# Optimization experiments

Hardware: AMD Instinct MI355X
Metric: run time of the kernel (lower is better)

The kernel has to match this reference:

```python
import jax, jax.numpy as jnp
import numpy as np
import math

B, N, D = 4, 1024, 1024
H = 16
HD = D // H          # 64
TOP_K = 64
NUM_STATIC = 32


def setup_inputs() -> dict:
    key = jax.random.key(0)
    ks = jax.random.split(key, 10)
    s = 1.0 / math.sqrt(D)  # ~ nn.Linear default init scale
    inp = {
        "x": jax.random.normal(ks[0], (B, N, D), dtype=jnp.float32),
        "Wq": jax.random.uniform(ks[1], (D, D), jnp.float32, -s, s),
        "bq": jax.random.uniform(ks[2], (D,), jnp.float32, -s, s),
        "Wk": jax.random.uniform(ks[3], (D, D), jnp.float32, -s, s),
        "bk": jax.random.uniform(ks[4], (D,), jnp.float32, -s, s),
        "Wv": jax.random.uniform(ks[5], (D, D), jnp.float32, -s, s),
        "bv": jax.random.uniform(ks[6], (D,), jnp.float32, -s, s),
        "Wo": jax.random.uniform(ks[7], (D, D), jnp.float32, -s, s),
        "bo": jax.random.uniform(ks[8], (D,), jnp.float32, -s, s),
        "static_keys": jax.random.normal(ks[9], (NUM_STATIC, D), dtype=jnp.float32),
    }
    return inp


def _heads(t):
    # [B, N, D] -> [B, H, N, HD]
    return t.reshape(B, N, H, HD).transpose(0, 2, 1, 3)


def reference(x, Wq, bq, Wk, bk, Wv, bv, Wo, bo, static_keys):
    Q = _heads(x @ Wq.T + bq)
    K = _heads(x @ Wk.T + bk)
    V = _heads(x @ Wv.T + bv)

    # Replace the first NUM_STATIC key slots with learned static keys.
    K_stat = static_keys.reshape(1, NUM_STATIC, H, HD).transpose(0, 2, 1, 3)  # [1,H,S,HD]
    K_stat = jnp.broadcast_to(K_stat, (B, H, NUM_STATIC, HD))
    K = jnp.concatenate([K_stat, K[:, :, NUM_STATIC:, :]], axis=2)  # [B,H,N,HD]

    scores = jnp.einsum("bhnd,bhmd->bhnm", Q, K) / math.sqrt(HD)  # [B,H,N,N]

    # top-k mask: keep top_k scores per query, -inf elsewhere
    top_scores, top_idx = jax.lax.top_k(scores, TOP_K)  # [B,H,N,K]
    bi = jnp.arange(B)[:, None, None, None]
    hi = jnp.arange(H)[None, :, None, None]
    ni = jnp.arange(N)[None, None, :, None]
    masked = jnp.full(scores.shape, -jnp.inf, dtype=scores.dtype)
    masked = masked.at[bi, hi, ni, top_idx].set(top_scores)

    attn = jax.nn.softmax(masked, axis=-1)
    out = jnp.einsum("bhnm,bhmd->bhnd", attn, V)  # [B,H,N,HD]
    out = out.transpose(0, 2, 1, 3).reshape(B, N, D)
    return out @ Wo.T + bo
```

## Files before the change

kernel.cpp:

```cpp
#include <hip/hip_runtime.h>

#define NSTAT 32
#define MAXSEL 76

typedef __attribute__((ext_vector_type(8))) short bf16x8_t;
typedef __attribute__((ext_vector_type(4))) float f32x4_t;

#define GLOAD_LDS16(g, l) \
    __builtin_amdgcn_global_load_lds((const __attribute__((address_space(1))) void*)(g), \
                                     (__attribute__((address_space(3))) void*)(l), 16, 0, 0)

__device__ __forceinline__ ushort rtn_bf16(float a) {
    unsigned u = __float_as_uint(a);
    return (ushort)((u + 0x7FFFu + ((u >> 16) & 1u)) >> 16);
}
__device__ __forceinline__ void limb2(float a, ushort& h, ushort& l) {
    ushort hh = rtn_bf16(a);
    float fh = __uint_as_float(((unsigned)hh) << 16);
    float r1 = a - fh;
    l = rtn_bf16(r1);
    h = hh;
}

__global__ __launch_bounds__(256)
void decomp_w_kernel(const float* __restrict__ Wq, const float* __restrict__ Wk,
                     const float* __restrict__ Wv, const float* __restrict__ Wo,
                     ushort* __restrict__ WLq, ushort* __restrict__ WoLb)
{
    const int m = blockIdx.y;
    const float* src = (m == 0) ? Wq : (m == 1) ? Wk : (m == 2) ? Wv : Wo;
    const int idx = blockIdx.x * 256 + threadIdx.x;
    const int e8 = idx * 8;
    const int row = e8 >> 10, k0 = e8 & 1023;
    const int kt = k0 >> 5, q = (k0 >> 3) & 3;
    const size_t doff = ((size_t)row << 10) + (size_t)(kt * 32) + (size_t)((q ^ (row & 3)) * 8);

    float4 v0 = *(const float4*)(src + e8);
    float4 v1 = *(const float4*)(src + e8 + 4);
    float f[8] = {v0.x, v0.y, v0.z, v0.w, v1.x, v1.y, v1.z, v1.w};

    const size_t Mi = (size_t)1 << 20;
    ushort h[8], l[8];
    #pragma unroll
    for (int e = 0; e < 8; ++e) limb2(f[e], h[e], l[e]);
    ushort* H = (m == 3) ? WoLb : WLq + (size_t)(m * 2) * Mi;
    ushort* L = H + Mi;
    *(ushort4*)(H + doff)     = make_ushort4(h[0],h[1],h[2],h[3]);
    *(ushort4*)(H + doff + 4) = make_ushort4(h[4],h[5],h[6],h[7]);
    *(ushort4*)(L + doff)     = make_ushort4(l[0],l[1],l[2],l[3]);
    *(ushort4*)(L + doff + 4) = make_ushort4(l[4],l[5],l[6],l[7]);
}

__global__ __launch_bounds__(256, 3)
void limb_gemm_kernel(const float* __restrict__ A,
                      const ushort* __restrict__ WLq, const ushort* __restrict__ WoLb,
                      const float* __restrict__ bq, const float* __restrict__ bk,
                      const float* __restrict__ bv, const float* __restrict__ bo,
                      const float* __restrict__ statk,
                      float* __restrict__ Qw, float* __restrict__ Vw,
                      ushort* __restrict__ KHo, ushort* __restrict__ KLo,
                      float* __restrict__ Cout, int is_out)
{
    __shared__ __align__(16) ushort Al[2][128][32];
    __shared__ __align__(16) ushort Bl[2][2][128][32];

    const int t = threadIdx.x;
    const int bx = blockIdx.x, by = blockIdx.y;
    const int mode = is_out ? 3 : (int)blockIdx.z;
    const int wc0 = bx * 128;
    const int arow0 = by * 128;

    const size_t Mi = (size_t)1 << 20;
    const ushort* BpH;
    const float* bias;
    if (mode == 0)      { BpH = WLq;          bias = bq; }
    else if (mode == 1) { BpH = WLq + 2*Mi;   bias = bk; }
    else if (mode == 2) { BpH = WLq + 4*Mi;   bias = bv; }
    else                { BpH = WoLb;         bias = bo; }
    const ushort* BpL = BpH + Mi;

    const int ll = t & 63, w = t >> 6;

    f32x4_t acc[4][4];
    #pragma unroll
    for (int i = 0; i < 4; ++i)
        #pragma unroll
        for (int j = 0; j < 4; ++j) acc[i][j] = (f32x4_t){0.f, 0.f, 0.f, 0.f};

    auto stageB = [&](int kt, int bb) {
        #pragma unroll
        for (int limb = 0; limb < 2; ++limb) {
            const ushort* src = limb ? BpL : BpH;
            #pragma unroll
            for (int call = 0; call < 2; ++call) {
                int chunk = (w * 2 + call) * 64 + ll;
                int eoff = chunk * 8;
                int row = eoff >> 5, qp = (eoff >> 3) & 3;
                const ushort* g = src + ((size_t)(wc0 + row) << 10) + kt * 32 + qp * 8;
                char* l = ((char*)&Bl[bb][limb][0][0]) + (w * 2 + call) * 1024;
                GLOAD_LDS16(g, l);
            }
        }
    };
    const int srow = t >> 1, skh = (t & 1) * 16;
    auto loadA = [&](int kt, float4* a4) {
        const float* p = A + (((size_t)(arow0 + srow)) << 10) + kt * 32 + skh;
        a4[0] = *(const float4*)(p + 0);
        a4[1] = *(const float4*)(p + 4);
        a4[2] = *(const float4*)(p + 8);
        a4[3] = *(const float4*)(p + 12);
    };
    auto writeA = [&](const float4* a4) {
        float f[16];
        #pragma unroll
        for (int i = 0; i < 4; ++i) {
            f[i*4+0] = a4[i].x; f[i*4+1] = a4[i].y; f[i*4+2] = a4[i].z; f[i*4+3] = a4[i].w;
        }
        ushort h[16], lo[16];
        #pragma unroll
        for (int e = 0; e < 16; ++e) limb2(f[e], h[e], lo[e]);
        const int sw = srow & 3;
        #pragma unroll
        for (int qq = 0; qq < 2; ++qq) {
            int q = (skh >> 3) + qq;
            int qo = (q ^ sw) * 8;
            bf16x8_t vH, vL;
            #pragma unroll
            for (int e = 0; e < 8; ++e) {
                vH[e] = (short)h[qq*8+e]; vL[e] = (short)lo[qq*8+e];
            }
            *(bf16x8_t*)&Al[0][srow][qo] = vH;
            *(bf16x8_t*)&Al[1][srow][qo] = vL;
        }
    };

    const int wr = (w >> 1) * 64, wcv = (w & 1) * 64;
    const int fr = ll & 15, kg = ll >> 4;

    auto compute = [&](int bb) {
        bf16x8_t af[4][2];
        #pragma unroll
        for (int i = 0; i < 4; ++i) {
            int row = wr + i * 16 + fr;
            int qo = (kg ^ (row & 3)) * 8;
            af[i][0] = *(const bf16x8_t*)&Al[0][row][qo];
            af[i][1] = *(const bf16x8_t*)&Al[1][row][qo];
        }
        #pragma unroll
        for (int j = 0; j < 4; ++j) {
            int row = wcv + j * 16 + fr;
            int qo = (kg ^ (row & 3)) * 8;
            bf16x8_t b0 = *(const bf16x8_t*)&Bl[bb][0][row][qo];
            bf16x8_t b1 = *(const bf16x8_t*)&Bl[bb][1][row][qo];
            #pragma unroll
            for (int i = 0; i < 4; ++i) {
                acc[i][j] = __builtin_amdgcn_mfma_f32_16x16x32_bf16(af[i][0], b0, acc[i][j], 0, 0, 0);
                acc[i][j] = __builtin_amdgcn_mfma_f32_16x16x32_bf16(af[i][0], b1, acc[i][j], 0, 0, 0);
                acc[i][j] = __builtin_amdgcn_mfma_f32_16x16x32_bf16(af[i][1], b0, acc[i][j], 0, 0, 0);
            }
        }
    };

    float4 a4[4];
    loadA(0, a4);
    writeA(a4);
    stageB(0, 0);
    __syncthreads();

    float4 a4n[4];
    for (int kt = 0; kt < 32; ++kt) {
        int bb = kt & 1;
        if (kt < 31) {
            stageB(kt + 1, bb ^ 1);
            loadA(kt + 1, a4n);
        }
        compute(bb);
        __syncthreads();
        if (kt < 31) writeA(a4n);
        __syncthreads();
    }

    #pragma unroll
    for (int i = 0; i < 4; ++i) {
        #pragma unroll
        for (int j = 0; j < 4; ++j) {
            int c = wc0 + wcv + j * 16 + (ll & 15);
            float bv_ = bias[c];
            #pragma unroll
            for (int q = 0; q < 4; ++q) {
                int gr = arow0 + wr + i * 16 + (kg) * 4 + q;
                float v = acc[i][j][q] + bv_;
                if (mode == 3) {
                    Cout[(size_t)gr * 1024 + c] = v;
                } else {
                    int b = gr >> 10, n = gr & 1023;
                    int h = c >> 6, d = c & 63;
                    size_t bhn = ((size_t)(b * 16 + h)) * 1024 + n;
                    if (mode == 1) {
                        if (n < NSTAT) v = statk[n * 1024 + c];
                        ushort kh, klo;
                        limb2(v, kh, klo);
                        size_t off = bhn * 64 + (size_t)(((d >> 3) ^ (n & 7)) * 8) + (d & 7);
                        KHo[off] = kh;
                        KLo[off] = klo;
                    } else {
                        float* Out = (mode == 0) ? Qw : Vw;
                        Out[bhn * 64 + d] = v;
                    }
                }
            }
        }
    }
}

__device__ __forceinline__ void radix_stage7(int* __restrict__ hist, int r, int l,
                                             const unsigned* __restrict__ ku,
                                             unsigned pref, unsigned mask, int shift,
                                             int tgt, int2* __restrict__ piv)
{
    #pragma unroll
    for (int b = 0; b < 8; ++b) hist[(l*8 + b)*33 + r] = 0;
    __syncthreads();
    #pragma unroll
    for (int j = 0; j < 64; ++j) {
        unsigned k = ku[j];
        if ((k & mask) == pref)
            atomicAdd(&hist[(int)((k >> shift) & 127u)*33 + r], 1);
    }
    __syncthreads();
    int seg = 0;
    #pragma unroll
    for (int b = 0; b < 8; ++b) seg += hist[(l*8 + b)*33 + r];
    int suf = seg;
    #pragma unroll
    for (int off = 1; off < 16; off <<= 1) {
        int v = __shfl_down(suf, off, 16);
        suf += (l + off < 16) ? v : 0;
    }
    const int above = suf - seg;
    if (above < tgt && above + seg >= tgt) {
        int c = above;
        #pragma unroll
        for (int b = 7; b >= 0; --b) {
            int h = hist[(l*8 + b)*33 + r];
            if (c + h >= tgt) { piv[r] = make_int2(l*8 + b, tgt - c); break; }
            c += h;
        }
    }
    __syncthreads();
}

__global__ __launch_bounds__(512, 4)
void attn_mfma_kernel(const float* __restrict__ Qw,
                      const ushort* __restrict__ KH, const ushort* __restrict__ KL,
                      const float* __restrict__ Vw, float* __restrict__ outp)
{
    __shared__ __align__(16) char pool[58368];
    __shared__ int2 piv[32];
    __shared__ int cnt[32];
    __shared__ float rowsum[32];

    ushort* Klds0 = (ushort*)pool;
    ushort* Klds1 = Klds0 + 8192;
    int* hist = (int*)pool;
    float (*Qs)[68]  = (float(*)[68])(pool + 32768);
    float (*sc)[132] = (float(*)[132])(pool + 41472);
    uint2 (*sel)[MAXSEL] = (uint2(*)[MAXSEL])(pool + 32768);

    const int t = threadIdx.x;
    const int bid0 = blockIdx.x;
    const int bid = (bid0 & 7) * 256 + (bid0 >> 3);
    const int qt = bid & 31;
    const int bh = bid >> 5;
    const int n0 = qt * 32;
    const float* Qbase = Qw + ((size_t)bh * 1024 + n0) * 64;
    const float* Vbase = Vw + (size_t)bh * 1024 * 64;
    const ushort* KHb = KH + (size_t)bh * 1024 * 64;
    const ushort* KLb = KL + (size_t)bh * 1024 * 64;

    const int ll = t & 63;
    const int w  = t >> 6;
    const int qh = w >> 2;
    const int kr = w & 3;
    const int r  = t >> 4, l = t & 15;

    {
        int q = t >> 4, dq = (t & 15) * 4;
        *(float4*)&Qs[q][dq] = *(const float4*)(Qbase + q * 64 + dq);
    }
    auto stageK = [&](int c) {
        const size_t cb = (size_t)c * 8192;
        #pragma unroll
        for (int i = 0; i < 2; ++i) {
            int boff = i * 8192 + w * 1024;
            GLOAD_LDS16(KHb + cb + boff / 2 + ll * 8, ((char*)Klds0) + boff);
            GLOAD_LDS16(KLb + cb + boff / 2 + ll * 8, ((char*)Klds1) + boff);
        }
    };
    stageK(0);
    if (t < 32) cnt[t] = 0;
    __syncthreads();

    bf16x8_t aH[2], aL[2];
    {
        const int arow = qh * 16 + (ll & 15), akg = ll >> 4;
        #pragma unroll
        for (int s = 0; s < 2; ++s) {
            const float* qp = &Qs[arow][s*32 + akg*8];
            float4 q0 = *(const float4*)qp;
            float4 q1 = *(const float4*)(qp + 4);
            float qv[8] = {q0.x,q0.y,q0.z,q0.w,q1.x,q1.y,q1.z,q1.w};
            #pragma unroll
            for (int j = 0; j < 8; ++j) {
                ushort hh, lo2;
                limb2(qv[j], hh, lo2);
                aH[s][j] = (short)hh; aL[s][j] = (short)lo2;
            }
        }
    }
    __syncthreads();

    unsigned ku[64];

    #pragma unroll
    for (int c = 0; c < 8; ++c) {
        #pragma unroll
        for (int tile = 0; tile < 2; ++tile) {
            const int m0 = kr * 32 + tile * 16;
            const int brow = m0 + (ll & 15);
            f32x4_t a_ = {0.f, 0.f, 0.f, 0.f};
            #pragma unroll
            for (int s = 0; s < 2; ++s) {
                int q2 = (s*4 + (ll >> 4)) ^ (brow & 7);
                int off = brow*64 + q2*8;
                bf16x8_t bH = *(const bf16x8_t*)&Klds0[off];
                bf16x8_t bL = *(const bf16x8_t*)&Klds1[off];
                a_ = __builtin_amdgcn_mfma_f32_16x16x32_bf16(aH[s], bH, a_, 0, 0, 0);
                a_ = __builtin_amdgcn_mfma_f32_16x16x32_bf16(aH[s], bL, a_, 0, 0, 0);
                a_ = __builtin_amdgcn_mfma_f32_16x16x32_bf16(aL[s], bH, a_, 0, 0, 0);
            }
            const int qr = qh * 16 + (ll >> 4) * 4;
            const int mcol = m0 + (ll & 15);
            sc[qr+0][mcol] = a_[0];
            sc[qr+1][mcol] = a_[1];
            sc[qr+2][mcol] = a_[2];
            sc[qr+3][mcol] = a_[3];
        }
        __syncthreads();

        if (c < 7) stageK(c + 1);
        {
            float4 v0 = *(const float4*)&sc[r][l*8];
            float4 v1 = *(const float4*)&sc[r][l*8 + 4];
            float vv[8] = {v0.x,v0.y,v0.z,v0.w,v1.x,v1.y,v1.z,v1.w};
            #pragma unroll
            for (int e = 0; e < 8; ++e) {
                float vc = fminf(fmaxf(vv[e], -31.9f), 31.9f);
                ku[c*8 + e] = (unsigned)(int)fmaf(vc, 32768.f, 1048576.f);
            }
        }
        __syncthreads();
    }

    int tgt = 64;
    radix_stage7(hist, r, l, ku, 0u, 0u, 14, tgt, piv);
    unsigned pref = (unsigned)piv[r].x << 14; tgt = piv[r].y;
    radix_stage7(hist, r, l, ku, pref, 0x1FC000u, 7, tgt, piv);
    pref |= (unsigned)piv[r].x << 7; tgt = piv[r].y;
    radix_stage7(hist, r, l, ku, pref, 0x1FFF80u, 0, tgt, piv);
    const unsigned thr = pref | (unsigned)piv[r].x;

    const unsigned bhi = thr + 2u;
    const unsigned blo = thr - 2u;
    #pragma unroll
    for (int j = 0; j < 64; ++j) {
        unsigned k = ku[j];
        if (k >= blo) {
            int slot = atomicAdd(&cnt[r], 1);
            if (slot < MAXSEL)
                sel[r][slot] = make_uint2((unsigned)((j >> 3)*128 + l*8 + (j & 7)), k);
        }
    }
    __syncthreads();

    {
        int cc = cnt[r]; cc = (cc < MAXSEL) ? cc : MAXSEL;
        int Dl = 0, ml = 0;
        for (int j = l; j < cc; j += 16) {
            unsigned k = sel[r][j].y;
            if (k > bhi) Dl++; else ml++;
        }
        #pragma unroll
        for (int off = 8; off; off >>= 1) {
            Dl += __shfl_xor(Dl, off, 16);
            ml += __shfl_xor(ml, off, 16);
        }
        const float frac = (float)(64 - Dl) / (float)ml;
        float ls = 0.f;
        for (int j = l; j < cc; j += 16) {
            uint2 p = sel[r][j];
            float wgt = __expf((float)(int)(p.y - thr) * 3.814697265625e-6f);
            if (p.y <= bhi) wgt *= frac;
            p.y = __float_as_uint(wgt);
            sel[r][j] = p;
            ls += wgt;
        }
        #pragma unroll
        for (int off = 8; off; off >>= 1) ls += __shfl_xor(ls, off, 16);
        if (l == 0) { rowsum[r] = ls; cnt[r] = cc; }
    }
    __syncthreads();

    {
        const int pr = t >> 4;
        const int d4 = (t & 15) * 4;
        const int bb = bh >> 4, hh = bh & 15;
        const int cc = cnt[pr];
        float4 a = make_float4(0.f, 0.f, 0.f, 0.f);
        int j = 0;
        for (; j + 1 < cc; j += 2) {
            uint2 p0 = sel[pr][j];
            uint2 p1 = sel[pr][j+1];
            float w0 = __uint_as_float(p0.y);
            float w1 = __uint_as_float(p1.y);
            float4 v0 = *(const float4*)(Vbase + (size_t)p0.x * 64 + d4);
            float4 v1 = *(const float4*)(Vbase + (size_t)p1.x * 64 + d4);
            a.x += w0 * v0.x + w1 * v1.x;
            a.y += w0 * v0.y + w1 * v1.y;
            a.z += w0 * v0.z + w1 * v1.z;
            a.w += w0 * v0.w + w1 * v1.w;
        }
        if (j < cc) {
            uint2 p = sel[pr][j];
            float wv = __uint_as_float(p.y);
            float4 v = *(const float4*)(Vbase + (size_t)p.x * 64 + d4);
            a.x += wv * v.x; a.y += wv * v.y; a.z += wv * v.z; a.w += wv * v.w;
        }
        float inv = 1.0f / rowsum[pr];
        a.x *= inv; a.y *= inv; a.z *= inv; a.w *= inv;
        *(float4*)(outp + ((size_t)bb * 1024 + (n0 + pr)) * 1024 + hh * 64 + d4) = a;
    }
}

extern "C" void kernel_launch(void* const* d_in, const int* in_sizes, int n_in,
                              void* d_out, int out_size, void* d_ws, size_t ws_size,
                              hipStream_t stream) {
    const float* x     = (const float*)d_in[0];
    const float* Wq    = (const float*)d_in[1];
    const float* bq    = (const float*)d_in[2];
    const float* Wk    = (const float*)d_in[3];
    const float* bk    = (const float*)d_in[4];
    const float* Wv    = (const float*)d_in[5];
    const float* bv    = (const float*)d_in[6];
    const float* Wo    = (const float*)d_in[7];
    const float* bo    = (const float*)d_in[8];
    const float* statk = (const float*)d_in[9];
    float* out = (float*)d_out;
    char* base = (char*)d_ws;

    const size_t MiB = (size_t)1 << 20;
    float*  Qw   = (float*)(base);
    float*  Vw   = (float*)(base + 16*MiB);
    ushort* KH   = (ushort*)(base + 32*MiB);
    ushort* KL   = (ushort*)(base + 40*MiB);
    ushort* WoLb = (ushort*)(base + 48*MiB);
    ushort* WLq  = (ushort*)(base + 52*MiB);
    float*  op   = (float*)(base + 52*MiB);

    dim3 gd(512, 4);
    decomp_w_kernel<<<gd, 256, 0, stream>>>(Wq, Wk, Wv, Wo, WLq, WoLb);

    dim3 g1(8, 32, 3);
    limb_gemm_kernel<<<g1, 256, 0, stream>>>(x, WLq, WoLb, bq, bk, bv, bo, statk,
                                             Qw, Vw, KH, KL, nullptr, 0);

    attn_mfma_kernel<<<2048, 512, 0, stream>>>(Qw, KH, KL, Vw, op);

    dim3 g2(8, 32);
    limb_gemm_kernel<<<g2, 256, 0, stream>>>(op, WLq, WoLb, bq, bk, bv, bo, statk,
                                             Qw, Vw, KH, KL, out, 1);
}
```

Baseline: 293.1 us.

## Halve attention query tile to 16 rows, doubling blocks and threads per row

Each attention block now handles 16 queries instead of 32, so the grid grows to 4096 blocks and 32 threads cooperate on each row's radix select, with half the keys per thread. This cuts per-thread register use (the key array drops from 64 to 32 entries) and LDS, so more blocks fit per CU. The weighted V accumulation is split across two half-groups and combined with a shuffle. In exchange, every K chunk is loaded from global memory twice as often per query, which raises K traffic and the per-block fixed overhead.

```diff
diff --git a/kernel.cpp b/kernel.cpp
--- a/kernel.cpp
+++ b/kernel.cpp
@@ -213,16 +213,16 @@
     }
 }
 
-__device__ __forceinline__ void radix_stage7(int* __restrict__ hist, int r, int l,
+__device__ __forceinline__ void radix_stage4(int* __restrict__ hist, int r, int l2,
                                              const unsigned* __restrict__ ku,
                                              unsigned pref, unsigned mask, int shift,
                                              int tgt, int2* __restrict__ piv)
 {
     #pragma unroll
-    for (int b = 0; b < 8; ++b) hist[(l*8 + b)*33 + r] = 0;
-    __syncthreads();
-    #pragma unroll
-    for (int j = 0; j < 64; ++j) {
+    for (int b = 0; b < 4; ++b) hist[(l2*4 + b)*33 + r] = 0;
+    __syncthreads();
+    #pragma unroll
+    for (int j = 0; j < 32; ++j) {
         unsigned k = ku[j];
         if ((k & mask) == pref)
             atomicAdd(&hist[(int)((k >> shift) & 127u)*33 + r], 1);
@@ -230,20 +230,20 @@
     __syncthreads();
     int seg = 0;
     #pragma unroll
-    for (int b = 0; b < 8; ++b) seg += hist[(l*8 + b)*33 + r];
+    for (int b = 0; b < 4; ++b) seg += hist[(l2*4 + b)*33 + r];
     int suf = seg;
     #pragma unroll
-    for (int off = 1; off < 16; off <<= 1) {
-        int v = __shfl_down(suf, off, 16);
-        suf += (l + off < 16) ? v : 0;
+    for (int off = 1; off < 32; off <<= 1) {
+        int v = __shfl_down(suf, off, 32);
+        suf += (l2 + off < 32) ? v : 0;
     }
     const int above = suf - seg;
     if (above < tgt && above + seg >= tgt) {
         int c = above;
         #pragma unroll
-        for (int b = 7; b >= 0; --b) {
-            int h = hist[(l*8 + b)*33 + r];
-            if (c + h >= tgt) { piv[r] = make_int2(l*8 + b, tgt - c); break; }
+        for (int b = 3; b >= 0; --b) {
+            int h = hist[(l2*4 + b)*33 + r];
+            if (c + h >= tgt) { piv[r] = make_int2(l2*4 + b, tgt - c); break; }
             c += h;
         }
     }
@@ -255,24 +255,24 @@
                       const ushort* __restrict__ KH, const ushort* __restrict__ KL,
                       const float* __restrict__ Vw, float* __restrict__ outp)
 {
-    __shared__ __align__(16) char pool[58368];
-    __shared__ int2 piv[32];
-    __shared__ int cnt[32];
-    __shared__ float rowsum[32];
+    __shared__ __align__(16) char pool[45568];
+    __shared__ int2 piv[16];
+    __shared__ int cnt[16];
+    __shared__ float rowsum[16];
 
     ushort* Klds0 = (ushort*)pool;
     ushort* Klds1 = Klds0 + 8192;
     int* hist = (int*)pool;
     float (*Qs)[68]  = (float(*)[68])(pool + 32768);
-    float (*sc)[132] = (float(*)[132])(pool + 41472);
+    float (*sc)[132] = (float(*)[132])(pool + 37120);
     uint2 (*sel)[MAXSEL] = (uint2(*)[MAXSEL])(pool + 32768);
 
     const int t = threadIdx.x;
     const int bid0 = blockIdx.x;
-    const int bid = (bid0 & 7) * 256 + (bid0 >> 3);
-    const int qt = bid & 31;
-    const int bh = bid >> 5;
-    const int n0 = qt * 32;
+    const int bid = (bid0 & 7) * 512 + (bid0 >> 3);
+    const int qt = bid & 63;
+    const int bh = bid >> 6;
+    const int n0 = qt * 16;
     const float* Qbase = Qw + ((size_t)bh * 1024 + n0) * 64;
     const float* Vbase = Vw + (size_t)bh * 1024 * 64;
     const ushort* KHb = KH + (size_t)bh * 1024 * 64;
@@ -280,11 +280,9 @@
 
     const int ll = t & 63;
     const int w  = t >> 6;
-    const int qh = w >> 2;
-    const int kr = w & 3;
-    const int r  = t >> 4, l = t & 15;
-
-    {
+    const int r  = t >> 5, l2 = t & 31;
+
+    if (t < 256) {
         int q = t >> 4, dq = (t & 15) * 4;
         *(float4*)&Qs[q][dq] = *(const float4*)(Qbase + q * 64 + dq);
     }
@@ -298,12 +296,12 @@
         }
     };
     stageK(0);
-    if (t < 32) cnt[t] = 0;
+    if (t < 16) cnt[t] = 0;
     __syncthreads();
 
     bf16x8_t aH[2], aL[2];
     {
-        const int arow = qh * 16 + (ll & 15), akg = ll >> 4;
+        const int arow = ll & 15, akg = ll >> 4;
         #pragma unroll
         for (int s = 0; s < 2; ++s) {
             const float* qp = &Qs[arow][s*32 + akg*8];
@@ -320,14 +318,12 @@
     }
     __syncthreads();
 
-    unsigned ku[64];
+    unsigned ku[32];
 
     #pragma unroll
     for (int c = 0; c < 8; ++c) {
-        #pragma unroll
-        for (int tile = 0; tile < 2; ++tile) {
-            const int m0 = kr * 32 + tile * 16;
-            const int brow = m0 + (ll & 15);
+        {
+            const int brow = w * 16 + (ll & 15);
             f32x4_t a_ = {0.f, 0.f, 0.f, 0.f};
             #pragma unroll
             for (int s = 0; s < 2; ++s) {
@@ -339,46 +335,44 @@
                 a_ = __builtin_amdgcn_mfma_f32_16x16x32_bf16(aH[s], bL, a_, 0, 0, 0);
                 a_ = __builtin_amdgcn_mfma_f32_16x16x32_bf16(aL[s], bH, a_, 0, 0, 0);
             }
-            const int qr = qh * 16 + (ll >> 4) * 4;
-            const int mcol = m0 + (ll & 15);
-            sc[qr+0][mcol] = a_[0];
-            sc[qr+1][mcol] = a_[1];
-            sc[qr+2][mcol] = a_[2];
-            sc[qr+3][mcol] = a_[3];
+            const int qr = (ll >> 4) * 4;
+            sc[qr+0][brow] = a_[0];
+            sc[qr+1][brow] = a_[1];
+            sc[qr+2][brow] = a_[2];
+            sc[qr+3][brow] = a_[3];
         }
         __syncthreads();
 
         if (c < 7) stageK(c + 1);
         {
-            float4 v0 = *(const float4*)&sc[r][l*8];
-            float4 v1 = *(const float4*)&sc[r][l*8 + 4];
-            float vv[8] = {v0.x,v0.y,v0.z,v0.w,v1.x,v1.y,v1.z,v1.w};
-            #pragma unroll
-            for (int e = 0; e < 8; ++e) {
+            float4 v4 = *(const float4*)&sc[r][l2*4];
+            float vv[4] = {v4.x, v4.y, v4.z, v4.w};
+            #pragma unroll
+            for (int e = 0; e < 4; ++e) {
                 float vc = fminf(fmaxf(vv[e], -31.9f), 31.9f);
-                ku[c*8 + e] = (unsigned)(int)fmaf(vc, 32768.f, 1048576.f);
+                ku[c*4 + e] = (unsigned)(int)fmaf(vc, 32768.f, 1048576.f);
             }
         }
         __syncthreads();
     }
 
     int tgt = 64;
-    radix_stage7(hist, r, l, ku, 0u, 0u, 14, tgt, piv);
+    radix_stage4(hist, r, l2, ku, 0u, 0u, 14, tgt, piv);
     unsigned pref = (unsigned)piv[r].x << 14; tgt = piv[r].y;
-    radix_stage7(hist, r, l, ku, pref, 0x1FC000u, 7, tgt, piv);
+    radix_stage4(hist, r, l2, ku, pref, 0x1FC000u, 7, tgt, piv);
     pref |= (unsigned)piv[r].x << 7; tgt = piv[r].y;
-    radix_stage7(hist, r, l, ku, pref, 0x1FFF80u, 0, tgt, piv);
+    radix_stage4(hist, r, l2, ku, pref, 0x1FFF80u, 0, tgt, piv);
     const unsigned thr = pref | (unsigned)piv[r].x;
 
     const unsigned bhi = thr + 2u;
     const unsigned blo = thr - 2u;
     #pragma unroll
-    for (int j = 0; j < 64; ++j) {
+    for (int j = 0; j < 32; ++j) {
         unsigned k = ku[j];
         if (k >= blo) {
             int slot = atomicAdd(&cnt[r], 1);
             if (slot < MAXSEL)
-                sel[r][slot] = make_uint2((unsigned)((j >> 3)*128 + l*8 + (j & 7)), k);
+                sel[r][slot] = make_uint2((unsigned)((j >> 2)*128 + l2*4 + (j & 3)), k);
         }
     }
     __syncthreads();
@@ -386,18 +380,18 @@
     {
         int cc = cnt[r]; cc = (cc < MAXSEL) ? cc : MAXSEL;
         int Dl = 0, ml = 0;
-        for (int j = l; j < cc; j += 16) {
+        for (int j = l2; j < cc; j += 32) {
             unsigned k = sel[r][j].y;
             if (k > bhi) Dl++; else ml++;
         }
         #pragma unroll
-        for (int off = 8; off; off >>= 1) {
-            Dl += __shfl_xor(Dl, off, 16);
-            ml += __shfl_xor(ml, off, 16);
+        for (int off = 16; off; off >>= 1) {
+            Dl += __shfl_xor(Dl, off, 32);
+            ml += __shfl_xor(ml, off, 32);
         }
         const float frac = (float)(64 - Dl) / (float)ml;
         float ls = 0.f;
-        for (int j = l; j < cc; j += 16) {
+        for (int j = l2; j < cc; j += 32) {
             uint2 p = sel[r][j];
             float wgt = __expf((float)(int)(p.y - thr) * 3.814697265625e-6f);
             if (p.y <= bhi) wgt *= frac;
@@ -406,39 +400,33 @@
             ls += wgt;
         }
         #pragma unroll
-        for (int off = 8; off; off >>= 1) ls += __shfl_xor(ls, off, 16);
-        if (l == 0) { rowsum[r] = ls; cnt[r] = cc; }
+        for (int off = 16; off; off >>= 1) ls += __shfl_xor(ls, off, 32);
+        if (l2 == 0) { rowsum[r] = ls; cnt[r] = cc; }
     }
     __syncthreads();
 
     {
-        const int pr = t >> 4;
+        const int pr = t >> 5;
+        const int h2 = (t >> 4) & 1;
         const int d4 = (t & 15) * 4;
         const int bb = bh >> 4, hh = bh & 15;
         const int cc = cnt[pr];
         float4 a = make_float4(0.f, 0.f, 0.f, 0.f);
-        int j = 0;
-        for (; j + 1 < cc; j += 2) {
-            uint2 p0 = sel[pr][j];
-            uint2 p1 = sel[pr][j+1];
-            float w0 = __uint_as_float(p0.y);
-            float w1 = __uint_as_float(p1.y);
-            float4 v0 = *(const float4*)(Vbase + (size_t)p0.x * 64 + d4);
-            float4 v1 = *(const float4*)(Vbase + (size_t)p1.x * 64 + d4);
-            a.x += w0 * v0.x + w1 * v1.x;
-            a.y += w0 * v0.y + w1 * v1.y;
-            a.z += w0 * v0.z + w1 * v1.z;
-            a.w += w0 * v0.w + w1 * v1.w;
-        }
-        if (j < cc) {
+        for (int j = h2; j < cc; j += 2) {
             uint2 p = sel[pr][j];
             float wv = __uint_as_float(p.y);
             float4 v = *(const float4*)(Vbase + (size_t)p.x * 64 + d4);
             a.x += wv * v.x; a.y += wv * v.y; a.z += wv * v.z; a.w += wv * v.w;
         }
-        float inv = 1.0f / rowsum[pr];
-        a.x *= inv; a.y *= inv; a.z *= inv; a.w *= inv;
-        *(float4*)(outp + ((size_t)bb * 1024 + (n0 + pr)) * 1024 + hh * 64 + d4) = a;
+        a.x += __shfl_xor(a.x, 16);
+        a.y += __shfl_xor(a.y, 16);
+        a.z += __shfl_xor(a.z, 16);
+        a.w += __shfl_xor(a.w, 16);
+        if (h2 == 0) {
+            float inv = 1.0f / rowsum[pr];
+            a.x *= inv; a.y *= inv; a.z *= inv; a.w *= inv;
+            *(float4*)(outp + ((size_t)bb * 1024 + (n0 + pr)) * 1024 + hh * 64 + d4) = a;
+        }
     }
 }
 
@@ -474,7 +462,7 @@
     limb_gemm_kernel<<<g1, 256, 0, stream>>>(x, WLq, WoLb, bq, bk, bv, bo, statk,
                                              Qw, Vw, KH, KL, nullptr, 0);
 
-    attn_mfma_kernel<<<2048, 512, 0, stream>>>(Qw, KH, KL, Vw, op);
+    attn_mfma_kernel<<<4096, 512, 0, stream>>>(Qw, KH, KL, Vw, op);
 
     dim3 g2(8, 32);
     limb_gemm_kernel<<<g2, 256, 0, stream>>>(op, WLq, WoLb, bq, bk, bv, bo, statk,
```

After: 309.1 us. +5.5%, slower.
